# Kernel optimization log

Hardware: AMD Instinct MI355X
Metric: run time of the kernel (lower is better)

Reference implementation:

```python
import jax, jax.numpy as jnp
import numpy as np

EMBED_DIM = 1024
NUM_HEADS = 16
HEAD_DIM = EMBED_DIM // NUM_HEADS
STD = 0.02


def setup_inputs() -> dict:
    key = jax.random.key(0)
    k1, k2, k3 = jax.random.split(key, 3)
    B, S = 2, 2048
    inputs = jax.random.normal(k1, (B, S, EMBED_DIM), dtype=jnp.float32)
    # qkv projection: Linear(E, 3E); torch Linear weight is [out, in]
    w_qkv = jax.random.normal(k2, (3 * EMBED_DIM, EMBED_DIM), dtype=jnp.float32) * STD
    b_qkv = jnp.zeros((3 * EMBED_DIM,), dtype=jnp.float32)
    w_out = jax.random.normal(k3, (EMBED_DIM, EMBED_DIM), dtype=jnp.float32) * STD
    b_out = jnp.zeros((EMBED_DIM,), dtype=jnp.float32)
    return {"inputs": inputs, "w_qkv": w_qkv, "b_qkv": b_qkv, "w_out": w_out, "b_out": b_out}


def reference(inputs, w_qkv, b_qkv, w_out, b_out):
    B, S, E = inputs.shape
    qkv = inputs @ w_qkv.T + b_qkv                      # [B,S,3E]
    q, k, v = jnp.split(qkv, 3, axis=2)                 # each [B,S,E]

    def split_heads(t):
        return t.reshape(B, S, NUM_HEADS, HEAD_DIM).transpose(0, 2, 1, 3)  # [B,H,S,D]

    q, k, v = split_heads(q), split_heads(k), split_heads(v)
    scores = jnp.einsum('bhqd,bhkd->bhqk', q, k) * (1.0 / np.sqrt(HEAD_DIM))
    causal = jnp.tril(jnp.ones((S, S), dtype=bool))     # [S,S]
    scores = jnp.where(causal[None, None, :, :], scores, -jnp.inf)
    probs = jax.nn.softmax(scores, axis=-1)             # dropout is identity in eval mode
    ctx = jnp.einsum('bhqk,bhkd->bhqd', probs, v)       # [B,H,S,D]
    ctx = ctx.transpose(0, 2, 1, 3).reshape(B, S, E)
    return ctx @ w_out.T + b_out
```

## Files before the change

### kernel.cpp

```cpp
#include <hip/hip_runtime.h>
#include <hip/hip_bf16.h>

#define BATCH 2
#define SEQ   2048
#define EMB   1024
#define NHEAD 16
#define HDIM  64
#define MTOT  (BATCH*SEQ)
#define KTOT  EMB

#define NX  (MTOT*EMB)
#define NW1 (3*EMB*EMB)
#define NW2 (EMB*EMB)

typedef short bf8 __attribute__((ext_vector_type(8)));
typedef short s4v __attribute__((ext_vector_type(4)));
typedef float f4  __attribute__((ext_vector_type(4)));
typedef unsigned int uint;

__device__ __forceinline__ short f2b(float f) {
    __hip_bfloat16 h = __float2bfloat16(f);
    return __builtin_bit_cast(short, h);
}
__device__ __forceinline__ void gl_lds16(const short* g, short* l) {
    __builtin_amdgcn_global_load_lds(
        (const __attribute__((address_space(1))) uint*)g,
        (__attribute__((address_space(3))) uint*)l, 16, 0, 0);
}
#define SWZ_SRC(lane)      ((((lane) ^ ((lane)>>2) ^ ((lane)>>4)) & 3) * 8)
#define SWZ_RD(quad, l16)  ((((quad) ^ (l16) ^ ((l16)>>2)) & 3) * 8)

__global__ __launch_bounds__(256) void cvt_all(
    const float* __restrict__ X, const float* __restrict__ W1,
    const float* __restrict__ W2,
    short* __restrict__ xb, short* __restrict__ w1b, short* __restrict__ w2b)
{
    int i4 = (blockIdx.x * 256 + threadIdx.x) * 4;
    const float* src; short* dst; int off;
    if (i4 < NX)            { src = X;  dst = xb;  off = i4; }
    else if (i4 < NX + NW1) { src = W1; dst = w1b; off = i4 - NX; }
    else                    { src = W2; dst = w2b; off = i4 - NX - NW1; }
    float4 v = *(const float4*)&src[off];
    s4v o; o[0]=f2b(v.x); o[1]=f2b(v.y); o[2]=f2b(v.z); o[3]=f2b(v.w);
    *(s4v*)&dst[off] = o;
}

#define GEMM_PROLOG(Aptr, Bptr) \
    __shared__ __align__(16) short As[128*32]; \
    __shared__ __align__(16) short Bs[128*32]; \
    const int tid  = threadIdx.x; \
    const int lane = tid & 63; \
    const int w    = tid >> 6; \
    const int l16  = lane & 15, quad = lane >> 4; \
    const int wm   = (w >> 1) * 64, wn = (w & 1) * 64; \
    const int srow = (lane >> 2); \
    const int scol = SWZ_SRC(lane); \
    f4 acc[4][4] = {}; \
    for (int k0 = 0; k0 < KTOT; k0 += 32) { \
        _Pragma("unroll") \
        for (int t = 0; t < 2; t++) { \
            int ra = blockIdx.x*128 + w*32 + t*16 + srow; \
            gl_lds16(&Aptr[(size_t)ra*KTOT + k0 + scol], &As[(w*32 + t*16)*32]); \
            int rb = blockIdx.y*128 + w*32 + t*16 + srow; \
            gl_lds16(&Bptr[(size_t)rb*KTOT + k0 + scol], &Bs[(w*32 + t*16)*32]); \
        } \
        __syncthreads(); \
        bf8 af[4], bf[4]; \
        _Pragma("unroll") \
        for (int i = 0; i < 4; i++) { \
            af[i] = *(const bf8*)&As[(wm + i*16 + l16)*32 + SWZ_RD(quad, l16)]; \
            bf[i] = *(const bf8*)&Bs[(wn + i*16 + l16)*32 + SWZ_RD(quad, l16)]; \
        } \
        _Pragma("unroll") \
        for (int mt = 0; mt < 4; mt++) \
            _Pragma("unroll") \
            for (int nt = 0; nt < 4; nt++) \
                acc[mt][nt] = __builtin_amdgcn_mfma_f32_16x16x32_bf16(af[mt], bf[nt], acc[mt][nt], 0, 0, 0); \
        __syncthreads(); \
    }

__global__ __launch_bounds__(256) void gemm_qkv(
    const short* __restrict__ Xb, const short* __restrict__ Wb,
    const float* __restrict__ bias,
    short* __restrict__ qb, short* __restrict__ kb, short* __restrict__ vtb)
{
    GEMM_PROLOG(Xb, Wb)
    #pragma unroll
    for (int mt = 0; mt < 4; mt++)
    #pragma unroll
    for (int nt = 0; nt < 4; nt++) {
        int colg = blockIdx.y*128 + wn + nt*16 + l16;
        float bv = bias[colg];
        #pragma unroll
        for (int r = 0; r < 4; r++) {
            int rowg = blockIdx.x*128 + wm + mt*16 + quad*4 + r;
            short h = f2b(acc[mt][nt][r] + bv);
            int bb = rowg >> 11, s = rowg & 2047;
            if (colg < 1024) {
                int hh = colg >> 6, d = colg & 63;
                qb[(((bb*NHEAD + hh)*SEQ + s) << 6) + d] = h;
            } else if (colg < 2048) {
                int c2 = colg - 1024, hh = c2 >> 6, d = c2 & 63;
                kb[(((bb*NHEAD + hh)*SEQ + s) << 6) + d] = h;
            } else {
                int c3 = colg - 2048, hh = c3 >> 6, d = c3 & 63;
                int ssw = (s & ~63) | (((s & 15) << 2) | ((s >> 4) & 3));
                vtb[((bb*NHEAD + hh)*HDIM + d)*SEQ + ssw] = h;
            }
        }
    }
}

__global__ __launch_bounds__(256, 4) void attn(
    const short* __restrict__ qb, const short* __restrict__ kb,
    const short* __restrict__ vtb, short* __restrict__ ctx)
{
    __shared__ __align__(16) short Ks[2*2*64*32];
    __shared__ __align__(16) short Vs[2*2*64*32];
    __shared__ __align__(16) short pl[4][16*64];
    const int tid = threadIdx.x;
    const int w = tid >> 6, lane = tid & 63;
    const int l16 = lane & 15, quad = lane >> 4;
    const int f  = blockIdx.x;
    const int bh = ((f & 7) << 2) + ((f >> 3) & 3);
    const int tq = 31 - (f >> 5);
    const int q0w = tq*64 + w*16;
    const int base = bh * (SEQ*HDIM);
    short* myp = pl[w];
    const float SC = 0.125f * 1.44269504f;

    const int lq  = lane >> 2;
    const int lsw = SWZ_SRC(lane);

    bf8 qa[2];
    #pragma unroll
    for (int kc = 0; kc < 2; kc++)
        qa[kc] = *(const bf8*)&qb[base + (q0w + l16)*HDIM + kc*32 + quad*8];

    f4 o[4] = {};
    float lacc[4] = {};
    const int lastj = q0w + 15;
    const int jmax  = tq*64 + 64;

    auto dma_stage = [&](int j0, int b) {
        #pragma unroll
        for (int tt = 0; tt < 4; tt++) {
            const int t = w*4 + tt;
            const int cc = t & 1, g = (t >> 1) & 3;
            if (t < 8) {
                gl_lds16(&kb[base + (j0 + g*16 + lq)*HDIM + cc*32 + lsw],
                         &Ks[b*4096 + (cc*64 + g*16)*32]);
            } else {
                gl_lds16(&vtb[base + (g*16 + lq)*SEQ + j0 + cc*32 + lsw],
                         &Vs[b*4096 + (cc*64 + g*16)*32]);
            }
        }
    };

    dma_stage(0, 0);
    __syncthreads();
    int buf = 0;
    for (int j0 = 0; j0 < jmax; j0 += 64) {
        if (j0 + 64 < jmax) dma_stage(j0 + 64, buf ^ 1);
        if (j0 <= lastj) {
            f4 s[4] = {};
            #pragma unroll
            for (int kf = 0; kf < 4; kf++)
                #pragma unroll
                for (int c = 0; c < 2; c++) {
                    bf8 kfr = *(const bf8*)&Ks[buf*4096 + (c*64 + kf*16 + l16)*32 + SWZ_RD(quad, l16)];
                    s[kf] = __builtin_amdgcn_mfma_f32_16x16x32_bf16(qa[c], kfr, s[kf], 0, 0, 0);
                }
            const bool needmask = (j0 + 63 > q0w);
            #pragma unroll
            for (int r = 0; r < 4; r++) {
                const int row = quad*4 + r;
                const int qi  = q0w + row;
                float e[4];
                #pragma unroll
                for (int kf = 0; kf < 4; kf++) {
                    e[kf] = __builtin_amdgcn_exp2f(s[kf][r] * SC);
                    if (needmask && (j0 + kf*16 + l16 > qi)) e[kf] = 0.0f;
                    lacc[r] += e[kf];
                }
                uint u01 = __builtin_amdgcn_perm(__builtin_bit_cast(uint, e[1]),
                                                 __builtin_bit_cast(uint, e[0]), 0x07060302u);
                uint u23 = __builtin_amdgcn_perm(__builtin_bit_cast(uint, e[3]),
                                                 __builtin_bit_cast(uint, e[2]), 0x07060302u);
                uint2 pk = {u01, u23};
                int c8 = ((l16 >> 1) ^ (row & 7));
                *(uint2*)&myp[row*64 + c8*8 + (l16 & 1)*4] = pk;
            }
            asm volatile("" ::: "memory");
            bf8 pa[2];
            #pragma unroll
            for (int kc = 0; kc < 2; kc++)
                pa[kc] = *(const bf8*)&myp[l16*64 + (((kc*4 + quad) ^ (l16 & 7)))*8];
            #pragma unroll
            for (int dt = 0; dt < 4; dt++)
                #pragma unroll
                for (int c = 0; c < 2; c++) {
                    bf8 vf = *(const bf8*)&Vs[buf*4096 + (c*64 + dt*16 + l16)*32 + SWZ_RD(quad, l16)];
                    o[dt] = __builtin_amdgcn_mfma_f32_16x16x32_bf16(pa[c], vf, o[dt], 0, 0, 0);
                }
        }
        __syncthreads();
        buf ^= 1;
    }
    #pragma unroll
    for (int r = 0; r < 4; r++) {
        float v = lacc[r];
        v += __shfl_xor(v, 1);
        v += __shfl_xor(v, 2);
        v += __shfl_xor(v, 4);
        v += __shfl_xor(v, 8);
        lacc[r] = v;
    }
    const int b = bh >> 4, h = bh & 15;
    #pragma unroll
    for (int r = 0; r < 4; r++) {
        float inv = 1.0f / lacc[r];
        int qi = q0w + quad*4 + r;
        int rowoff = (b*SEQ + qi)*EMB + h*HDIM;
        #pragma unroll
        for (int dt = 0; dt < 4; dt++)
            ctx[rowoff + dt*16 + l16] = f2b(o[dt][r] * inv);
    }
}

__global__ __launch_bounds__(256) void gemm_out(
    const short* __restrict__ A, const short* __restrict__ Wb,
    const float* __restrict__ bias, float* __restrict__ out)
{
    GEMM_PROLOG(A, Wb)
    #pragma unroll
    for (int mt = 0; mt < 4; mt++)
    #pragma unroll
    for (int nt = 0; nt < 4; nt++) {
        int colg = blockIdx.y*128 + wn + nt*16 + l16;
        float bv = bias[colg];
        #pragma unroll
        for (int r = 0; r < 4; r++) {
            int rowg = blockIdx.x*128 + wm + mt*16 + quad*4 + r;
            out[(size_t)rowg*EMB + colg] = acc[mt][nt][r] + bv;
        }
    }
}

extern "C" void kernel_launch(void* const* d_in, const int* in_sizes, int n_in,
                              void* d_out, int out_size, void* d_ws, size_t ws_size,
                              hipStream_t stream) {
    const float* X    = (const float*)d_in[0];
    const float* Wqkv = (const float*)d_in[1];
    const float* Bqkv = (const float*)d_in[2];
    const float* Wout = (const float*)d_in[3];
    const float* Bout = (const float*)d_in[4];
    float* out = (float*)d_out;

    short* xb    = (short*)d_ws;
    short* w1b   = xb  + NX;
    short* w2b   = w1b + NW1;
    short* qb    = w2b + NW2;
    short* kb    = qb  + NX;
    short* vtb   = kb  + NX;
    short* ctx   = vtb + NX;

    cvt_all<<<(NX+NW1+NW2)/1024, 256, 0, stream>>>(X, Wqkv, Wout, xb, w1b, w2b);
    dim3 g1(MTOT/128, 3*EMB/128);
    gemm_qkv<<<g1, 256, 0, stream>>>(xb, w1b, Bqkv, qb, kb, vtb);
    attn<<<dim3(1024), 256, 0, stream>>>(qb, kb, vtb, ctx);
    dim3 g3(MTOT/128, EMB/128);
    gemm_out<<<g3, 256, 0, stream>>>(ctx, w2b, Bout, out);
}
```

Measured before the change: 183.2 us.

## Double-buffer LDS tiles in QKV and output GEMMs to overlap loads

Replaces the shared GEMM prologue macro with explicit double-buffered LDS staging in both projection GEMMs. The next K-tile is loaded asynchronously while the MFMAs run on the current buffer, which removes one barrier per iteration. The output GEMM also widens each stage to 64 K-elements. Together these aim to hide global-to-LDS latency. The cost is doubled (or quadrupled) LDS use per block, which can lower occupancy.

```diff
diff --git a/kernel.cpp b/kernel.cpp
--- a/kernel.cpp
+++ b/kernel.cpp
@@ -45,46 +45,51 @@
     *(s4v*)&dst[off] = o;
 }
 
-#define GEMM_PROLOG(Aptr, Bptr) \
-    __shared__ __align__(16) short As[128*32]; \
-    __shared__ __align__(16) short Bs[128*32]; \
-    const int tid  = threadIdx.x; \
-    const int lane = tid & 63; \
-    const int w    = tid >> 6; \
-    const int l16  = lane & 15, quad = lane >> 4; \
-    const int wm   = (w >> 1) * 64, wn = (w & 1) * 64; \
-    const int srow = (lane >> 2); \
-    const int scol = SWZ_SRC(lane); \
-    f4 acc[4][4] = {}; \
-    for (int k0 = 0; k0 < KTOT; k0 += 32) { \
-        _Pragma("unroll") \
-        for (int t = 0; t < 2; t++) { \
-            int ra = blockIdx.x*128 + w*32 + t*16 + srow; \
-            gl_lds16(&Aptr[(size_t)ra*KTOT + k0 + scol], &As[(w*32 + t*16)*32]); \
-            int rb = blockIdx.y*128 + w*32 + t*16 + srow; \
-            gl_lds16(&Bptr[(size_t)rb*KTOT + k0 + scol], &Bs[(w*32 + t*16)*32]); \
-        } \
-        __syncthreads(); \
-        bf8 af[4], bf[4]; \
-        _Pragma("unroll") \
-        for (int i = 0; i < 4; i++) { \
-            af[i] = *(const bf8*)&As[(wm + i*16 + l16)*32 + SWZ_RD(quad, l16)]; \
-            bf[i] = *(const bf8*)&Bs[(wn + i*16 + l16)*32 + SWZ_RD(quad, l16)]; \
-        } \
-        _Pragma("unroll") \
-        for (int mt = 0; mt < 4; mt++) \
-            _Pragma("unroll") \
-            for (int nt = 0; nt < 4; nt++) \
-                acc[mt][nt] = __builtin_amdgcn_mfma_f32_16x16x32_bf16(af[mt], bf[nt], acc[mt][nt], 0, 0, 0); \
-        __syncthreads(); \
-    }
-
 __global__ __launch_bounds__(256) void gemm_qkv(
     const short* __restrict__ Xb, const short* __restrict__ Wb,
     const float* __restrict__ bias,
     short* __restrict__ qb, short* __restrict__ kb, short* __restrict__ vtb)
 {
-    GEMM_PROLOG(Xb, Wb)
+    __shared__ __align__(16) short As[2][128*32];
+    __shared__ __align__(16) short Bs[2][128*32];
+    const int tid  = threadIdx.x;
+    const int lane = tid & 63;
+    const int w    = tid >> 6;
+    const int l16  = lane & 15, quad = lane >> 4;
+    const int wm   = (w >> 1) * 64, wn = (w & 1) * 64;
+    const int srow = (lane >> 2);
+    const int scol = SWZ_SRC(lane);
+    f4 acc[4][4] = {};
+
+    auto stage = [&](int k0, int b) {
+        #pragma unroll
+        for (int t = 0; t < 2; t++) {
+            int ra = blockIdx.x*128 + w*32 + t*16 + srow;
+            gl_lds16(&Xb[(size_t)ra*KTOT + k0 + scol], &As[b][(w*32 + t*16)*32]);
+            int rb = blockIdx.y*128 + w*32 + t*16 + srow;
+            gl_lds16(&Wb[(size_t)rb*KTOT + k0 + scol], &Bs[b][(w*32 + t*16)*32]);
+        }
+    };
+
+    stage(0, 0);
+    __syncthreads();
+    int buf = 0;
+    for (int k0 = 0; k0 < KTOT; k0 += 32) {
+        if (k0 + 32 < KTOT) stage(k0 + 32, buf ^ 1);
+        bf8 af[4], bf[4];
+        #pragma unroll
+        for (int i = 0; i < 4; i++) {
+            af[i] = *(const bf8*)&As[buf][(wm + i*16 + l16)*32 + SWZ_RD(quad, l16)];
+            bf[i] = *(const bf8*)&Bs[buf][(wn + i*16 + l16)*32 + SWZ_RD(quad, l16)];
+        }
+        #pragma unroll
+        for (int mt = 0; mt < 4; mt++)
+            #pragma unroll
+            for (int nt = 0; nt < 4; nt++)
+                acc[mt][nt] = __builtin_amdgcn_mfma_f32_16x16x32_bf16(af[mt], bf[nt], acc[mt][nt], 0, 0, 0);
+        __syncthreads();
+        buf ^= 1;
+    }
     #pragma unroll
     for (int mt = 0; mt < 4; mt++)
     #pragma unroll
@@ -232,7 +237,51 @@
     const short* __restrict__ A, const short* __restrict__ Wb,
     const float* __restrict__ bias, float* __restrict__ out)
 {
-    GEMM_PROLOG(A, Wb)
+    __shared__ __align__(16) short As[2][2*128*32];
+    __shared__ __align__(16) short Bs[2][2*128*32];
+    const int tid  = threadIdx.x;
+    const int lane = tid & 63;
+    const int w    = tid >> 6;
+    const int l16  = lane & 15, quad = lane >> 4;
+    const int wm   = (w >> 1) * 64, wn = (w & 1) * 64;
+    const int srow = (lane >> 2);
+    const int scol = SWZ_SRC(lane);
+    f4 acc[4][4] = {};
+
+    auto stage = [&](int k0, int b) {
+        #pragma unroll
+        for (int t = 0; t < 4; t++) {
+            const int rr = w*32 + (t & 1)*16;
+            const int kc = t >> 1;
+            int ra = blockIdx.x*128 + rr + srow;
+            gl_lds16(&A[(size_t)ra*KTOT + k0 + kc*32 + scol],  &As[b][kc*4096 + rr*32]);
+            int rb = blockIdx.y*128 + rr + srow;
+            gl_lds16(&Wb[(size_t)rb*KTOT + k0 + kc*32 + scol], &Bs[b][kc*4096 + rr*32]);
+        }
+    };
+
+    stage(0, 0);
+    __syncthreads();
+    int buf = 0;
+    for (int k0 = 0; k0 < KTOT; k0 += 64) {
+        if (k0 + 64 < KTOT) stage(k0 + 64, buf ^ 1);
+        #pragma unroll
+        for (int kc = 0; kc < 2; kc++) {
+            bf8 af[4], bf[4];
+            #pragma unroll
+            for (int i = 0; i < 4; i++) {
+                af[i] = *(const bf8*)&As[buf][kc*4096 + (wm + i*16 + l16)*32 + SWZ_RD(quad, l16)];
+                bf[i] = *(const bf8*)&Bs[buf][kc*4096 + (wn + i*16 + l16)*32 + SWZ_RD(quad, l16)];
+            }
+            #pragma unroll
+            for (int mt = 0; mt < 4; mt++)
+                #pragma unroll
+                for (int nt = 0; nt < 4; nt++)
+                    acc[mt][nt] = __builtin_amdgcn_mfma_f32_16x16x32_bf16(af[mt], bf[nt], acc[mt][nt], 0, 0, 0);
+        }
+        __syncthreads();
+        buf ^= 1;
+    }
     #pragma unroll
     for (int mt = 0; mt < 4; mt++)
     #pragma unroll
```

Result: slower. 186.9 us (+2.0%).
